# Kernel tuning notes

Measured on AMD Instinct MI355X. Metric: run time of the kernel, lower is better.

The kernel has to match this reference:

```python
import jax, jax.numpy as jnp
import numpy as np

N, E, F_IN, F_E, H = 50000, 800000, 128, 16, 64
NEG_SLOPE = 0.2


def _glorot(key, shape):
    fan_in, fan_out = shape[0], shape[-1]
    lim = np.sqrt(6.0 / (fan_in + fan_out))
    return jax.random.uniform(key, shape, jnp.float32, -lim, lim)


def setup_inputs() -> dict:
    key = jax.random.key(0)
    ks = jax.random.split(key, 24)
    inp = {
        "x": jax.random.normal(ks[0], (N, F_IN), jnp.float32),
        "edge_index": jax.random.randint(ks[1], (2, E), 0, N, jnp.int64),
        "edge_attr": jax.random.normal(ks[2], (E, F_E), jnp.float32),
    }
    k = 3
    for i, f_in in zip((1, 2, 3), (F_IN, H, H)):
        inp[f"W{i}"] = _glorot(ks[k], (f_in, H)); k += 1
        inp[f"as{i}"] = _glorot(ks[k], (H,)); k += 1
        inp[f"ad{i}"] = _glorot(ks[k], (H,)); k += 1
        inp[f"We{i}"] = _glorot(ks[k], (F_E, H)); k += 1
        inp[f"ae{i}"] = _glorot(ks[k], (H,)); k += 1
        inp[f"b{i}"] = jnp.zeros((H,), jnp.float32)
        k += 1
    return inp


def gat_conv(x, src, dst, ea, W, a_s, a_d, We, a_e, b):
    # x: [N, f_in]; src/dst: [E'] (self-loops already appended); ea: [E', F_E]
    n = x.shape[0]
    h = x @ W                                   # [N, H]
    alpha_src = h @ a_s                          # [N]
    alpha_dst = h @ a_d                          # [N]
    alpha_e = (ea @ We) @ a_e                    # [E']
    alpha = alpha_src[src] + alpha_dst[dst] + alpha_e
    alpha = jnp.where(alpha > 0, alpha, NEG_SLOPE * alpha)  # leaky_relu
    # segment softmax over incoming edges of each dst node
    amax = jax.ops.segment_max(alpha, dst, num_segments=n)
    ex = jnp.exp(alpha - amax[dst])
    denom = jax.ops.segment_sum(ex, dst, num_segments=n)
    coef = ex / (denom[dst] + 1e-16)             # [E']
    out = jax.ops.segment_sum(h[src] * coef[:, None], dst, num_segments=n)
    return out + b


def reference(x, edge_index, edge_attr,
              W1, as1, ad1, We1, ae1, b1,
              W2, as2, ad2, We2, ae2, b2,
              W3, as3, ad3, We3, ae3, b3):
    n = x.shape[0]
    # add self-loops (PyG GATConv default), edge_attr fill_value='mean'
    loop = jnp.arange(n, dtype=edge_index.dtype)
    src = jnp.concatenate([edge_index[0], loop])
    dst = jnp.concatenate([edge_index[1], loop])
    ea_mean = jnp.mean(edge_attr, axis=0)
    ea = jnp.concatenate([edge_attr, jnp.broadcast_to(ea_mean, (n, edge_attr.shape[1]))], axis=0)

    x1 = jax.nn.elu(gat_conv(x, src, dst, ea, W1, as1, ad1, We1, ae1, b1))
    x2 = jax.nn.elu(gat_conv(x1, src, dst, ea, W2, as2, ad2, We2, ae2, b2))
    x3 = jax.nn.elu(gat_conv(x2, src, dst, ea, W3, as3, ad3, We3, ae3, b3))
    node_embeddings = x1 + x2 + x3
    graph_embedding = jnp.mean(node_embeddings, axis=0, keepdims=True)  # batch=None path
    return node_embeddings, graph_embedding
```

## Files before the change

### kernel.cpp

```cpp
#include <hip/hip_runtime.h>
#include <hip/hip_fp16.h>
#include <math.h>

#define HD 64
#define MAXNBK 256

typedef unsigned long long u64;
typedef _Float16 f16;
typedef _Float16 f16x8 __attribute__((ext_vector_type(8)));
typedef float f32x4 __attribute__((ext_vector_type(4)));

__device__ __forceinline__ u64 pack_rec(int src, float a0, float a1, float a2) {
    return (u64)(src & 0xFFFF)
         | ((u64)__half_as_ushort(__float2half(a0)) << 16)
         | ((u64)__half_as_ushort(__float2half(a1)) << 32)
         | ((u64)__half_as_ushort(__float2half(a2)) << 48);
}

__global__ void k_init(int* cnt, int* bcnt, float* gacc, int N, int NBK) {
    int i = blockIdx.x * blockDim.x + threadIdx.x;
    if (i < N) cnt[i] = 0;
    if (i < NBK * 16) bcnt[i] = 0;
    if (i < HD) gacc[i] = 0.f;
}

__global__ void k_pre(const int* __restrict__ ei, const float* __restrict__ ea,
                      const float* We1, const float* ae1,
                      const float* We2, const float* ae2,
                      const float* We3, const float* ae3,
                      int E, int FE, int ntiles, int NBK,
                      int* cnt, int* bcnt, u64* __restrict__ recE,
                      float* __restrict__ partials) {
    extern __shared__ float lds[];
    float* sEA = lds;
    float* su = sEA + 256 * (FE + 1);
    float* colacc = su + 3 * FE;
    int* lcnt = (int*)(colacc + 256 * 4);
    int t = threadIdx.x;
    int ldE = FE + 1;

    if (t < 3 * FE) {
        int l = t / FE, f = t % FE;
        const float* We = (l == 0) ? We1 : (l == 1) ? We2 : We3;
        const float* ae = (l == 0) ? ae1 : (l == 1) ? ae2 : ae3;
        float s = 0.f;
        for (int hh = 0; hh < HD; ++hh) s += We[f * HD + hh] * ae[hh];
        su[t] = s;
    }
    lcnt[t] = 0;

    const float4* ea4 = (const float4*)ea;
    size_t tot4 = (size_t)E * FE / 4;
    int per_tile4 = 64 * FE;
    float4 acc = make_float4(0.f, 0.f, 0.f, 0.f);

    for (int tile = blockIdx.x; tile < ntiles; tile += gridDim.x) {
        __syncthreads();
        size_t base4 = (size_t)tile * per_tile4;
        for (int i = t; i < per_tile4; i += 256) {
            size_t g4 = base4 + i;
            if (g4 < tot4) {
                float4 v = ea4[g4];
                acc.x += v.x; acc.y += v.y; acc.z += v.z; acc.w += v.w;
                int g = i * 4;
                int e_loc = g / FE, f = g % FE;
                float* p = &sEA[e_loc * ldE + f];
                p[0] = v.x; p[1] = v.y; p[2] = v.z; p[3] = v.w;
            }
        }
        __syncthreads();
        int e = tile * 256 + t;
        if (e < E) {
            float a0 = 0.f, a1 = 0.f, a2 = 0.f;
            const float* row = &sEA[t * ldE];
            for (int f = 0; f < FE; ++f) {
                float v = row[f];
                a0 += v * su[f];
                a1 += v * su[FE + f];
                a2 += v * su[2 * FE + f];
            }
            int src = ei[e], dst = ei[E + e];
            recE[e] = pack_rec(src, a0, a1, a2);
            atomicAdd(&cnt[dst], 1);
            atomicAdd(&lcnt[dst >> 8], 1);
        }
    }

    colacc[t * 4 + 0] = acc.x; colacc[t * 4 + 1] = acc.y;
    colacc[t * 4 + 2] = acc.z; colacc[t * 4 + 3] = acc.w;
    __syncthreads();
    if (t < NBK && lcnt[t]) atomicAdd(&bcnt[t * 16], lcnt[t]);
    if (t < 16) {
        int q = t >> 2, j = t & 3;
        float s = 0.f;
        for (int k = 0; k < 64; ++k) s += colacc[(q + k * 4) * 4 + j];
        partials[blockIdx.x * 16 + (q * 4 + j)] = s;
    }
}

__global__ void k_u2(const float* __restrict__ partials, int NB,
                     const float* We1, const float* ae1,
                     const float* We2, const float* ae2,
                     const float* We3, const float* ae3,
                     float* sE, int FE, float invE,
                     int* bcnt , int* bbase, int NBK, int E) {
    __shared__ float red[256];
    __shared__ float uu[64];
    __shared__ int bs[256];
    int t = threadIdx.x;
    if (t < 3 * FE) {
        int l = t / FE, f = t % FE;
        const float* We = (l == 0) ? We1 : (l == 1) ? We2 : We3;
        const float* ae = (l == 0) ? ae1 : (l == 1) ? ae2 : ae3;
        float s = 0.f;
        for (int hh = 0; hh < HD; ++hh) s += We[f * HD + hh] * ae[hh];
        uu[t] = s;
    }
    int col = t & 15, grp = t >> 4;
    float s = 0.f;
    for (int b = grp; b < NB; b += 16) s += partials[b * FE + col];
    red[t] = s;
    int v = (t < NBK) ? bcnt[t * 16] : 0;
    bs[t] = v;
    __syncthreads();
    for (int d = 1; d < 256; d <<= 1) {
        int x = (t >= d) ? bs[t - d] : 0;
        __syncthreads();
        bs[t] += x;
        __syncthreads();
    }
    int pre = bs[t] - v;
    if (t < NBK) { bbase[t] = pre; bcnt[t * 16] = pre; }
    if (t == 0) bbase[NBK] = E;
    if (t < 16) {
        float v2 = 0.f;
        for (int g = 0; g < 16; ++g) v2 += red[g * 16 + t];
        red[t] = v2 * invE;
    }
    __syncthreads();
    if (t < 3) {
        float a = 0.f;
        for (int f = 0; f < FE; ++f) a += red[f] * uu[t * FE + f];
        sE[t] = a;
    }
}

__global__ void k_scanA(const int* __restrict__ cnt, int* pre, int* blocksums, int N) {
    __shared__ int lds[256];
    int t = threadIdx.x;
    int n = blockIdx.x * 256 + t;
    int v = (n < N) ? cnt[n] + 1 : 0;
    lds[t] = v;
    __syncthreads();
    for (int d = 1; d < 256; d <<= 1) {
        int x = (t >= d) ? lds[t - d] : 0;
        __syncthreads();
        lds[t] += x;
        __syncthreads();
    }
    if (n < N) pre[n] = lds[t] - v;
    if (t == 255) blocksums[blockIdx.x] = lds[255];
}

__global__ void k_scanB(int* blocksums, int NBLK, int* total) {
    __shared__ int lds[256];
    int t = threadIdx.x;
    int v = (t < NBLK) ? blocksums[t] : 0;
    lds[t] = v;
    __syncthreads();
    for (int d = 1; d < 256; d <<= 1) {
        int x = (t >= d) ? lds[t - d] : 0;
        __syncthreads();
        lds[t] += x;
        __syncthreads();
    }
    if (t < NBLK) blocksums[t] = lds[t] - v;
    if (t == 255) *total = lds[255];
}

__global__ void k_scanC(const int* __restrict__ pre, const int* __restrict__ blocksums,
                        const int* __restrict__ total, int* row_ptr,
                        u64* __restrict__ rec, const float* __restrict__ sE, int N) {
    int n = blockIdx.x * 256 + threadIdx.x;
    if (n < N) {
        int r = pre[n] + blocksums[blockIdx.x];
        row_ptr[n] = r;
        rec[r] = pack_rec(n, sE[0], sE[1], sE[2]);
    }
    if (n == 0) row_ptr[N] = *total;
}

__global__ void k_bucket(const int* __restrict__ ei, const u64* __restrict__ recE,
                         int E, int chunk, int* bfill ,
                         u64* __restrict__ binned, unsigned char* __restrict__ bdstl,
                         int NBK) {
    __shared__ int lcnt[MAXNBK], gb[MAXNBK], lrank[MAXNBK];
    int t = threadIdx.x;
    lcnt[t] = 0;
    __syncthreads();
    int lo = blockIdx.x * chunk, hi = min(E, lo + chunk);
    for (int e = lo + t; e < hi; e += 256)
        atomicAdd(&lcnt[ei[E + e] >> 8], 1);
    __syncthreads();
    if (t < NBK) {
        lrank[t] = 0;
        gb[t] = lcnt[t] ? atomicAdd(&bfill[t * 16], lcnt[t]) : 0;
    }
    __syncthreads();
    for (int e = lo + t; e < hi; e += 256) {
        u64 r = recE[e];
        int dst = ei[E + e];
        int b = dst >> 8;
        int rank = atomicAdd(&lrank[b], 1);
        int pos = gb[b] + rank;
        binned[pos] = r;
        bdstl[pos] = (unsigned char)(dst & 255);
    }
}

__global__ void k_sort(const int* __restrict__ bbase, const int* __restrict__ row_ptr,
                       const u64* __restrict__ binned, const unsigned char* __restrict__ bdstl,
                       u64* __restrict__ rec, int N) {
    __shared__ int lfill[256];
    int b = blockIdx.x, t = threadIdx.x;
    int gnode = (b << 8) + t;
    lfill[t] = (gnode < N) ? row_ptr[gnode] + 1 : 0;
    __syncthreads();
    int base = bbase[b], nrec = bbase[b + 1] - base;
    for (int i = t; i < nrec; i += 256) {
        u64 r = binned[base + i];
        int dl = bdstl[base + i];
        int p = atomicAdd(&lfill[dl], 1);
        rec[p] = r;
    }
}

__global__ void k_gemm(const void* __restrict__ xin, int in_f16,
                       const float* __restrict__ W,
                       const float* __restrict__ a_s, const float* __restrict__ a_d,
                       __half* __restrict__ h, float* __restrict__ as_n,
                       float* __restrict__ ad_n, int N, int K) {
    extern __shared__ char smem[];
    const int SK = K + 8;
    f16* xs = (f16*)smem;
    f16* wt = xs + 64 * SK;
    int t = threadIdx.x;
    int nb = blockIdx.x * 64;

    int nK4 = K >> 2;
    if (in_f16) {
        const __half* xh = (const __half*)xin;
        for (int i = t; i < 64 * nK4; i += 256) {
            int row = i / nK4, c4 = i % nK4;
            int gr = nb + row; if (gr >= N) gr = N - 1;
            u64 v = ((const u64*)(xh + (size_t)gr * K))[c4];
            *(u64*)&xs[row * SK + c4 * 4] = v;
        }
    } else {
        const float* xf = (const float*)xin;
        for (int i = t; i < 64 * nK4; i += 256) {
            int row = i / nK4, c4 = i % nK4;
            int gr = nb + row; if (gr >= N) gr = N - 1;
            float4 v = ((const float4*)(xf + (size_t)gr * K))[c4];
            f16* p = &xs[row * SK + c4 * 4];
            p[0] = (f16)v.x; p[1] = (f16)v.y; p[2] = (f16)v.z; p[3] = (f16)v.w;
        }
    }
    for (int i = t; i < K * 64; i += 256) {
        int k = i >> 6, c = i & 63;
        wt[c * SK + k] = (f16)W[i];
    }
    __syncthreads();

    int wv = t >> 6, lane = t & 63;
    int m = lane & 15, quad = lane >> 4;
    int rowA = wv * 16 + m;

    f32x4 acc[4];
#pragma unroll
    for (int ct = 0; ct < 4; ++ct) acc[ct] = (f32x4){0.f, 0.f, 0.f, 0.f};

    for (int ks = 0; ks < (K >> 5); ++ks) {
        f16x8 a = *(const f16x8*)&xs[rowA * SK + ks * 32 + quad * 8];
#pragma unroll
        for (int ct = 0; ct < 4; ++ct) {
            f16x8 bf = *(const f16x8*)&wt[(ct * 16 + m) * SK + ks * 32 + quad * 8];
            acc[ct] = __builtin_amdgcn_mfma_f32_16x16x32_f16(a, bf, acc[ct], 0, 0, 0);
        }
    }

    __syncthreads();
    f16* ht = xs;
    const int HS = 72;
#pragma unroll
    for (int ct = 0; ct < 4; ++ct)
#pragma unroll
        for (int r = 0; r < 4; ++r) {
            int rl = wv * 16 + quad * 4 + r;
            ht[rl * HS + ct * 16 + m] = (f16)acc[ct][r];
        }
    __syncthreads();

    {
        int row = t >> 2, cb = (t & 3) * 16;
        int gr = nb + row;
        if (gr < N) {
            ulonglong2 v0 = *(const ulonglong2*)&ht[row * HS + cb];
            ulonglong2 v1 = *(const ulonglong2*)&ht[row * HS + cb + 8];
            *(ulonglong2*)(h + (size_t)gr * HD + cb) = v0;
            *(ulonglong2*)(h + (size_t)gr * HD + cb + 8) = v1;
        }
    }
    float ac = a_s[lane], adc = a_d[lane];
    for (int rr = 0; rr < 16; ++rr) {
        int row = wv * 16 + rr, gr = nb + row;
        float v = (float)ht[row * HS + lane];
        float vs = v * ac, vd = v * adc;
#pragma unroll
        for (int dd = 32; dd; dd >>= 1) {
            vs += __shfl_down(vs, dd, 64);
            vd += __shfl_down(vd, dd, 64);
        }
        if (lane == 0 && gr < N) { as_n[gr] = vs; ad_n[gr] = vd; }
    }
}

__global__ void k_aggr(const __half* __restrict__ h, const float* __restrict__ as_n,
                       const float* __restrict__ ad_n, const int* __restrict__ row_ptr,
                       const u64* __restrict__ rec, int l,
                       const float* __restrict__ b, __half* __restrict__ x_out,
                       float* __restrict__ emb, int N, int first) {
    int wave = threadIdx.x >> 6, lane = threadIdx.x & 63;
    int n = blockIdx.x * 4 + wave;
    if (n >= N) return;
    int base = row_ptr[n], end = row_ptr[n + 1];
    float adv = ad_n[n];
    const int shift = 16 * (l + 1);
    float m = -INFINITY, d = 0.f, acc = 0.f;

    for (int c = base; c < end; c += 64) {
        int cnt = min(64, end - c);
        float a = -INFINITY;
        int s = 0;
        if (lane < cnt) {
            u64 r = rec[c + lane];
            s = (int)(r & 0xFFFFull);
            float aE = __half2float(__ushort_as_half((unsigned short)(r >> shift)));
            a = as_n[s] + adv + aE;
            a = (a > 0.f) ? a : 0.2f * a;
        }
        float mc = a;
#pragma unroll
        for (int dd = 32; dd; dd >>= 1) mc = fmaxf(mc, __shfl_xor(mc, dd, 64));
        float mn = fmaxf(m, mc);
        float w = (lane < cnt) ? __expf(a - mn) : 0.f;
        float dc = w;
#pragma unroll
        for (int dd = 32; dd; dd >>= 1) dc += __shfl_xor(dc, dd, 64);
        float sc = __expf(m - mn);
        d = d * sc + dc;
        acc = acc * sc;
        m = mn;
        int j = 0;
        for (; j + 3 < cnt; j += 4) {
            int s0 = __shfl(s, j, 64), s1 = __shfl(s, j + 1, 64),
                s2 = __shfl(s, j + 2, 64), s3 = __shfl(s, j + 3, 64);
            float w0 = __shfl(w, j, 64), w1 = __shfl(w, j + 1, 64),
                  w2 = __shfl(w, j + 2, 64), w3 = __shfl(w, j + 3, 64);
            float h0 = __half2float(h[(size_t)s0 * HD + lane]);
            float h1 = __half2float(h[(size_t)s1 * HD + lane]);
            float h2 = __half2float(h[(size_t)s2 * HD + lane]);
            float h3 = __half2float(h[(size_t)s3 * HD + lane]);
            acc += w0 * h0; acc += w1 * h1; acc += w2 * h2; acc += w3 * h3;
        }
        for (; j < cnt; ++j) {
            int sj = __shfl(s, j, 64);
            float wj = __shfl(w, j, 64);
            acc += wj * __half2float(h[(size_t)sj * HD + lane]);
        }
    }

    float out = acc / (d + 1e-16f) + b[lane];
    float v = (out > 0.f) ? out : expm1f(out);
    x_out[(size_t)n * HD + lane] = __float2half(v);
    if (first) emb[(size_t)n * HD + lane] = v;
    else emb[(size_t)n * HD + lane] += v;
}

__global__ void k_red(const float* __restrict__ emb, float* gacc, int N) {
    __shared__ float lds[256];
    int f = threadIdx.x & 63, w = threadIdx.x >> 6;
    float s = 0.f;
    for (int n = blockIdx.x * 4 + w; n < N; n += gridDim.x * 4)
        s += emb[(size_t)n * HD + f];
    lds[threadIdx.x] = s;
    __syncthreads();
    if (w == 0) {
        float v = lds[f] + lds[64 + f] + lds[128 + f] + lds[192 + f];
        atomicAdd(&gacc[f], v);
    }
}

__global__ void k_div(const float* __restrict__ gacc, float* out, int N) {
    int f = threadIdx.x;
    if (f < HD) out[(size_t)N * HD + f] = gacc[f] / (float)N;
}

extern "C" void kernel_launch(void* const* d_in, const int* in_sizes, int n_in,
                              void* d_out, int out_size, void* d_ws, size_t ws_size,
                              hipStream_t stream) {
    const float* x = (const float*)d_in[0];
    const int* ei = (const int*)d_in[1];
    const float* ea = (const float*)d_in[2];

    const int FIN = in_sizes[3] / HD;
    const int N = in_sizes[0] / FIN;
    const int E = in_sizes[1] / 2;
    const int FE = in_sizes[2] / E;
    const int Ep = E + N;
    const int NBK = (N + 255) >> 8;
    const int NPRE = 512;

    const float* W[3];  const float* as_[3]; const float* ad_[3];
    const float* We[3]; const float* ae_[3]; const float* bb[3];
    for (int l = 0; l < 3; ++l) {
        W[l]  = (const float*)d_in[3 + 6 * l + 0];
        as_[l] = (const float*)d_in[3 + 6 * l + 1];
        ad_[l] = (const float*)d_in[3 + 6 * l + 2];
        We[l] = (const float*)d_in[3 + 6 * l + 3];
        ae_[l] = (const float*)d_in[3 + 6 * l + 4];
        bb[l] = (const float*)d_in[3 + 6 * l + 5];
    }

    int gN = (N + 255) / 256;
    int ntiles = (E + 255) / 256;
    int chunk = (E + NPRE - 1) / NPRE;

    char* ws = (char*)d_ws;
    size_t off = 0;
    auto alloc = [&](size_t bytes) {
        void* p = ws + off;
        off += (bytes + 255) & ~(size_t)255;
        return p;
    };
    __half* h      = (__half*)alloc((size_t)N * HD * 2);
    __half* x_cur  = (__half*)alloc((size_t)N * HD * 2);
    float*  as_n   = (float*)alloc((size_t)N * 4);
    float*  ad_n   = (float*)alloc((size_t)N * 4);
    int*    cnt    = (int*)alloc((size_t)N * 4);
    int*    rowp   = (int*)alloc((size_t)(N + 1) * 4);
    int*    pre    = (int*)alloc((size_t)N * 4);
    int*    bsums  = (int*)alloc(256 * 4);
    int*    total  = (int*)alloc(4);
    int*    bcnt   = (int*)alloc((size_t)MAXNBK * 16 * 4);
    int*    bbase  = (int*)alloc((size_t)(MAXNBK + 1) * 4);
    u64*    rec    = (u64*)alloc((size_t)Ep * 8);
    u64*    recE   = (u64*)alloc((size_t)E * 8);
    u64*    binned = (u64*)alloc((size_t)E * 8);
    unsigned char* bdstl = (unsigned char*)alloc((size_t)E);
    float*  partials = (float*)alloc((size_t)NPRE * FE * 4);
    float*  sE     = (float*)alloc(3 * 4);
    float*  gacc   = (float*)alloc(HD * 4);
    (void)ws_size; (void)n_in; (void)out_size;

    float* emb = (float*)d_out;

    k_init<<<gN, 256, 0, stream>>>(cnt, bcnt, gacc, N, NBK);
    size_t pre_lds = (size_t)(256 * (FE + 1) + 3 * FE + 256 * 4) * 4 + MAXNBK * 4;
    k_pre<<<NPRE, 256, pre_lds, stream>>>(ei, ea, We[0], ae_[0], We[1], ae_[1],
                                          We[2], ae_[2], E, FE, ntiles, NBK,
                                          cnt, bcnt, recE, partials);
    k_u2<<<1, 256, 0, stream>>>(partials, NPRE, We[0], ae_[0], We[1], ae_[1],
                                We[2], ae_[2], sE, FE, 1.0f / (float)E,
                                bcnt, bbase, NBK, E);
    k_scanA<<<gN, 256, 0, stream>>>(cnt, pre, bsums, N);
    k_scanB<<<1, 256, 0, stream>>>(bsums, gN, total);
    k_scanC<<<gN, 256, 0, stream>>>(pre, bsums, total, rowp, rec, sE, N);
    k_bucket<<<NPRE, 256, 0, stream>>>(ei, recE, E, chunk, bcnt, binned, bdstl, NBK);
    k_sort<<<NBK, 256, 0, stream>>>(bbase, rowp, binned, bdstl, rec, N);

    for (int l = 0; l < 3; ++l) {
        const void* xin = (l == 0) ? (const void*)x : (const void*)x_cur;
        int in_f16 = (l == 0) ? 0 : 1;
        int K = (l == 0) ? FIN : HD;
        size_t ldsz = (size_t)(2 * 64 * (K + 8)) * 2;
        k_gemm<<<(N + 63) / 64, 256, ldsz, stream>>>(xin, in_f16, W[l], as_[l], ad_[l],
                                                     h, as_n, ad_n, N, K);
        k_aggr<<<(N + 3) / 4, 256, 0, stream>>>(h, as_n, ad_n, rowp, rec, l,
                                                bb[l], x_cur, emb, N, (l == 0) ? 1 : 0);
    }

    k_red<<<256, 256, 0, stream>>>(emb, gacc, N);
    k_div<<<1, 64, 0, stream>>>(gacc, emb, N);
}
```

Baseline: 424.6 us.

## Derive bucket bases from node scan, one tile per block, wider gather unroll

```diff
diff --git a/kernel.cpp b/kernel.cpp
--- a/kernel.cpp
+++ b/kernel.cpp
@@ -17,10 +17,9 @@
          | ((u64)__half_as_ushort(__float2half(a2)) << 48);
 }
 
-__global__ void k_init(int* cnt, int* bcnt, float* gacc, int N, int NBK) {
+__global__ void k_init(int* cnt, float* gacc, int N) {
     int i = blockIdx.x * blockDim.x + threadIdx.x;
     if (i < N) cnt[i] = 0;
-    if (i < NBK * 16) bcnt[i] = 0;
     if (i < HD) gacc[i] = 0.f;
 }
 
@@ -28,14 +27,12 @@
                       const float* We1, const float* ae1,
                       const float* We2, const float* ae2,
                       const float* We3, const float* ae3,
-                      int E, int FE, int ntiles, int NBK,
-                      int* cnt, int* bcnt, u64* __restrict__ recE,
+                      int E, int FE, int* cnt, u64* __restrict__ recE,
                       float* __restrict__ partials) {
     extern __shared__ float lds[];
     float* sEA = lds;
     float* su = sEA + 256 * (FE + 1);
     float* colacc = su + 3 * FE;
-    int* lcnt = (int*)(colacc + 256 * 4);
     int t = threadIdx.x;
     int ldE = FE + 1;
 
@@ -47,49 +44,41 @@
         for (int hh = 0; hh < HD; ++hh) s += We[f * HD + hh] * ae[hh];
         su[t] = s;
     }
-    lcnt[t] = 0;
 
     const float4* ea4 = (const float4*)ea;
     size_t tot4 = (size_t)E * FE / 4;
     int per_tile4 = 64 * FE;
+    size_t base4 = (size_t)blockIdx.x * per_tile4;
     float4 acc = make_float4(0.f, 0.f, 0.f, 0.f);
-
-    for (int tile = blockIdx.x; tile < ntiles; tile += gridDim.x) {
-        __syncthreads();
-        size_t base4 = (size_t)tile * per_tile4;
-        for (int i = t; i < per_tile4; i += 256) {
-            size_t g4 = base4 + i;
-            if (g4 < tot4) {
-                float4 v = ea4[g4];
-                acc.x += v.x; acc.y += v.y; acc.z += v.z; acc.w += v.w;
-                int g = i * 4;
-                int e_loc = g / FE, f = g % FE;
-                float* p = &sEA[e_loc * ldE + f];
-                p[0] = v.x; p[1] = v.y; p[2] = v.z; p[3] = v.w;
-            }
-        }
-        __syncthreads();
-        int e = tile * 256 + t;
-        if (e < E) {
-            float a0 = 0.f, a1 = 0.f, a2 = 0.f;
-            const float* row = &sEA[t * ldE];
-            for (int f = 0; f < FE; ++f) {
-                float v = row[f];
-                a0 += v * su[f];
-                a1 += v * su[FE + f];
-                a2 += v * su[2 * FE + f];
-            }
-            int src = ei[e], dst = ei[E + e];
-            recE[e] = pack_rec(src, a0, a1, a2);
-            atomicAdd(&cnt[dst], 1);
-            atomicAdd(&lcnt[dst >> 8], 1);
-        }
-    }
-
+    for (int i = t; i < per_tile4; i += 256) {
+        size_t g4 = base4 + i;
+        if (g4 < tot4) {
+            float4 v = ea4[g4];
+            acc.x += v.x; acc.y += v.y; acc.z += v.z; acc.w += v.w;
+            int g = i * 4;
+            int e_loc = g / FE, f = g % FE;
+            float* p = &sEA[e_loc * ldE + f];
+            p[0] = v.x; p[1] = v.y; p[2] = v.z; p[3] = v.w;
+        }
+    }
     colacc[t * 4 + 0] = acc.x; colacc[t * 4 + 1] = acc.y;
     colacc[t * 4 + 2] = acc.z; colacc[t * 4 + 3] = acc.w;
     __syncthreads();
-    if (t < NBK && lcnt[t]) atomicAdd(&bcnt[t * 16], lcnt[t]);
+
+    int e = blockIdx.x * 256 + t;
+    if (e < E) {
+        float a0 = 0.f, a1 = 0.f, a2 = 0.f;
+        const float* row = &sEA[t * ldE];
+        for (int f = 0; f < FE; ++f) {
+            float v = row[f];
+            a0 += v * su[f];
+            a1 += v * su[FE + f];
+            a2 += v * su[2 * FE + f];
+        }
+        int src = ei[e], dst = ei[E + e];
+        recE[e] = pack_rec(src, a0, a1, a2);
+        atomicAdd(&cnt[dst], 1);
+    }
     if (t < 16) {
         int q = t >> 2, j = t & 3;
         float s = 0.f;
@@ -98,15 +87,49 @@
     }
 }
 
+__global__ void k_scanA(const int* __restrict__ cnt, int* pre, int* blocksums, int N) {
+    __shared__ int lds[256];
+    int t = threadIdx.x;
+    int n = blockIdx.x * 256 + t;
+    int v = (n < N) ? cnt[n] + 1 : 0;
+    lds[t] = v;
+    __syncthreads();
+    for (int d = 1; d < 256; d <<= 1) {
+        int x = (t >= d) ? lds[t - d] : 0;
+        __syncthreads();
+        lds[t] += x;
+        __syncthreads();
+    }
+    if (n < N) pre[n] = lds[t] - v;
+    if (t == 255) blocksums[blockIdx.x] = lds[255];
+}
+
+__global__ void k_scanB(int* blocksums, int NBLK, int* total) {
+    __shared__ int lds[256];
+    int t = threadIdx.x;
+    int v = (t < NBLK) ? blocksums[t] : 0;
+    lds[t] = v;
+    __syncthreads();
+    for (int d = 1; d < 256; d <<= 1) {
+        int x = (t >= d) ? lds[t - d] : 0;
+        __syncthreads();
+        lds[t] += x;
+        __syncthreads();
+    }
+    if (t < NBLK) blocksums[t] = lds[t] - v;
+    if (t == 255) *total = lds[255];
+}
+
 __global__ void k_u2(const float* __restrict__ partials, int NB,
                      const float* We1, const float* ae1,
                      const float* We2, const float* ae2,
                      const float* We3, const float* ae3,
                      float* sE, int FE, float invE,
-                     int* bcnt , int* bbase, int NBK, int E) {
-    __shared__ float red[256];
+                     const int* __restrict__ blocksums ,
+                     int* bfill , int* bbase, int NBK, int N, int E) {
+    __shared__ float red[256 * 4];
     __shared__ float uu[64];
-    __shared__ int bs[256];
+    __shared__ float mea[16];
     int t = threadIdx.x;
     if (t < 3 * FE) {
         int l = t / FE, f = t % FE;
@@ -116,66 +139,35 @@
         for (int hh = 0; hh < HD; ++hh) s += We[f * HD + hh] * ae[hh];
         uu[t] = s;
     }
-    int col = t & 15, grp = t >> 4;
-    float s = 0.f;
-    for (int b = grp; b < NB; b += 16) s += partials[b * FE + col];
-    red[t] = s;
-    int v = (t < NBK) ? bcnt[t * 16] : 0;
-    bs[t] = v;
-    __syncthreads();
-    for (int d = 1; d < 256; d <<= 1) {
-        int x = (t >= d) ? bs[t - d] : 0;
-        __syncthreads();
-        bs[t] += x;
-        __syncthreads();
-    }
-    int pre = bs[t] - v;
-    if (t < NBK) { bbase[t] = pre; bcnt[t * 16] = pre; }
+    const float4* p4 = (const float4*)partials;
+    int tot4 = NB * 4;
+    float4 acc = make_float4(0.f, 0.f, 0.f, 0.f);
+    for (int i = t; i < tot4; i += 256) {
+        float4 v = p4[i];
+        acc.x += v.x; acc.y += v.y; acc.z += v.z; acc.w += v.w;
+    }
+    red[t * 4 + 0] = acc.x; red[t * 4 + 1] = acc.y;
+    red[t * 4 + 2] = acc.z; red[t * 4 + 3] = acc.w;
+    if (t < NBK) {
+        int nb_before = min(t * 256, N);
+        int base = blocksums[t] - nb_before;
+        bbase[t] = base;
+        bfill[t * 16] = base;
+    }
     if (t == 0) bbase[NBK] = E;
+    __syncthreads();
     if (t < 16) {
-        float v2 = 0.f;
-        for (int g = 0; g < 16; ++g) v2 += red[g * 16 + t];
-        red[t] = v2 * invE;
+        int q = t >> 2, j = t & 3;
+        float s = 0.f;
+        for (int k = 0; k < 64; ++k) s += red[(q + k * 4) * 4 + j];
+        mea[q * 4 + j] = s * invE;
     }
     __syncthreads();
     if (t < 3) {
         float a = 0.f;
-        for (int f = 0; f < FE; ++f) a += red[f] * uu[t * FE + f];
+        for (int f = 0; f < FE; ++f) a += mea[f] * uu[t * FE + f];
         sE[t] = a;
     }
-}
-
-__global__ void k_scanA(const int* __restrict__ cnt, int* pre, int* blocksums, int N) {
-    __shared__ int lds[256];
-    int t = threadIdx.x;
-    int n = blockIdx.x * 256 + t;
-    int v = (n < N) ? cnt[n] + 1 : 0;
-    lds[t] = v;
-    __syncthreads();
-    for (int d = 1; d < 256; d <<= 1) {
-        int x = (t >= d) ? lds[t - d] : 0;
-        __syncthreads();
-        lds[t] += x;
-        __syncthreads();
-    }
-    if (n < N) pre[n] = lds[t] - v;
-    if (t == 255) blocksums[blockIdx.x] = lds[255];
-}
-
-__global__ void k_scanB(int* blocksums, int NBLK, int* total) {
-    __shared__ int lds[256];
-    int t = threadIdx.x;
-    int v = (t < NBLK) ? blocksums[t] : 0;
-    lds[t] = v;
-    __syncthreads();
-    for (int d = 1; d < 256; d <<= 1) {
-        int x = (t >= d) ? lds[t - d] : 0;
-        __syncthreads();
-        lds[t] += x;
-        __syncthreads();
-    }
-    if (t < NBLK) blocksums[t] = lds[t] - v;
-    if (t == 255) *total = lds[255];
 }
 
 __global__ void k_scanC(const int* __restrict__ pre, const int* __restrict__ blocksums,
@@ -362,6 +354,20 @@
         acc = acc * sc;
         m = mn;
         int j = 0;
+        for (; j + 7 < cnt; j += 8) {
+            int sx[8]; float wx[8];
+#pragma unroll
+            for (int q = 0; q < 8; ++q) {
+                sx[q] = __shfl(s, j + q, 64);
+                wx[q] = __shfl(w, j + q, 64);
+            }
+            float hx[8];
+#pragma unroll
+            for (int q = 0; q < 8; ++q)
+                hx[q] = __half2float(h[(size_t)sx[q] * HD + lane]);
+#pragma unroll
+            for (int q = 0; q < 8; ++q) acc += wx[q] * hx[q];
+        }
         for (; j + 3 < cnt; j += 4) {
             int s0 = __shfl(s, j, 64), s1 = __shfl(s, j + 1, 64),
                 s2 = __shfl(s, j + 2, 64), s3 = __shfl(s, j + 3, 64);
@@ -452,31 +458,30 @@
     int*    pre    = (int*)alloc((size_t)N * 4);
     int*    bsums  = (int*)alloc(256 * 4);
     int*    total  = (int*)alloc(4);
-    int*    bcnt   = (int*)alloc((size_t)MAXNBK * 16 * 4);
+    int*    bfill  = (int*)alloc((size_t)MAXNBK * 16 * 4);
     int*    bbase  = (int*)alloc((size_t)(MAXNBK + 1) * 4);
     u64*    rec    = (u64*)alloc((size_t)Ep * 8);
     u64*    recE   = (u64*)alloc((size_t)E * 8);
     u64*    binned = (u64*)alloc((size_t)E * 8);
     unsigned char* bdstl = (unsigned char*)alloc((size_t)E);
-    float*  partials = (float*)alloc((size_t)NPRE * FE * 4);
+    float*  partials = (float*)alloc((size_t)ntiles * 16 * 4);
     float*  sE     = (float*)alloc(3 * 4);
     float*  gacc   = (float*)alloc(HD * 4);
     (void)ws_size; (void)n_in; (void)out_size;
 
     float* emb = (float*)d_out;
 
-    k_init<<<gN, 256, 0, stream>>>(cnt, bcnt, gacc, N, NBK);
-    size_t pre_lds = (size_t)(256 * (FE + 1) + 3 * FE + 256 * 4) * 4 + MAXNBK * 4;
-    k_pre<<<NPRE, 256, pre_lds, stream>>>(ei, ea, We[0], ae_[0], We[1], ae_[1],
-                                          We[2], ae_[2], E, FE, ntiles, NBK,
-                                          cnt, bcnt, recE, partials);
-    k_u2<<<1, 256, 0, stream>>>(partials, NPRE, We[0], ae_[0], We[1], ae_[1],
-                                We[2], ae_[2], sE, FE, 1.0f / (float)E,
-                                bcnt, bbase, NBK, E);
+    k_init<<<gN, 256, 0, stream>>>(cnt, gacc, N);
+    size_t pre_lds = (size_t)(256 * (FE + 1) + 3 * FE + 256 * 4) * 4;
+    k_pre<<<ntiles, 256, pre_lds, stream>>>(ei, ea, We[0], ae_[0], We[1], ae_[1],
+                                            We[2], ae_[2], E, FE, cnt, recE, partials);
     k_scanA<<<gN, 256, 0, stream>>>(cnt, pre, bsums, N);
     k_scanB<<<1, 256, 0, stream>>>(bsums, gN, total);
+    k_u2<<<1, 256, 0, stream>>>(partials, ntiles, We[0], ae_[0], We[1], ae_[1],
+                                We[2], ae_[2], sE, FE, 1.0f / (float)E,
+                                bsums, bfill, bbase, NBK, N, E);
     k_scanC<<<gN, 256, 0, stream>>>(pre, bsums, total, rowp, rec, sE, N);
-    k_bucket<<<NPRE, 256, 0, stream>>>(ei, recE, E, chunk, bcnt, binned, bdstl, NBK);
+    k_bucket<<<NPRE, 256, 0, stream>>>(ei, recE, E, chunk, bfill, binned, bdstl, NBK);
     k_sort<<<NBK, 256, 0, stream>>>(bbase, rowp, binned, bdstl, rec, N);
 
     for (int l = 0; l < 3; ++l) {
```

New measurement: 413.4 us. 1.03x faster.
